# Kernel optimization log

Hardware: AMD Instinct MI355X
Metric: run time of the kernel (lower is better)

Reference implementation:

```python
import jax, jax.numpy as jnp
import numpy as np

N_SENT, B, S, D = 256, 512, 128, 1024
L, LATENT = 10331, 101  # int(sqrt(10331)) == 101


def setup_inputs() -> dict:
    key = jax.random.key(0)
    ks = jax.random.split(key, 16)
    inv = 1.0 / np.sqrt(D)
    return {
        'elmo_outputs': jax.random.normal(ks[0], (N_SENT, S, D), jnp.float32),
        'men_mask': jax.random.randint(ks[1], (B, S), 0, 2).astype(jnp.float32),
        'ctx_mask': jax.random.randint(ks[2], (B, S), 0, 2).astype(jnp.float32),
        'dist': jax.random.uniform(ks[3], (B, S), jnp.float32),
        'gathers': jax.random.randint(ks[4], (B,), 0, N_SENT),
        # nn.Linear weights, stored [out, in] as in torch
        'W_men_m': jax.random.normal(ks[5], (D, D), jnp.float32) * inv,
        'W_men_o': jax.random.normal(ks[6], (1, D), jnp.float32) * inv,
        'W_ctx_c': jax.random.normal(ks[7], (D, D), jnp.float32) * inv,
        'W_ctx_m': jax.random.normal(ks[8], (D, D), jnp.float32) * inv,
        'w_ctx_d': jax.random.normal(ks[9], (D,), jnp.float32),  # Linear(1, D) weight [D,1] squeezed
        'W_ctx_o': jax.random.normal(ks[10], (1, D), jnp.float32) * inv,
        'W_out': jax.random.normal(ks[11], (L, 2 * D), jnp.float32) * (1.0 / np.sqrt(2 * D)),
        'W_f2l': jax.random.normal(ks[12], (LATENT, 2 * D), jnp.float32) * (1.0 / np.sqrt(2 * D)),
        'W_l2l': jax.random.normal(ks[13], (L, LATENT), jnp.float32) * (1.0 / np.sqrt(LATENT)),
        'latent_scalar': jnp.array(0.1, jnp.float32),
    }


def reference(elmo_outputs, men_mask, ctx_mask, dist, gathers,
              W_men_m, W_men_o, W_ctx_c, W_ctx_m, w_ctx_d, W_ctx_o,
              W_out, W_f2l, W_l2l, latent_scalar):
    NEG = -10000.0
    # gather: sentence reps -> mention rows, [B, S, D]
    x = elmo_outputs[gathers]
    # mention additive attention
    men_h = jnp.tanh(jnp.einsum('bsd,ed->bse', x, W_men_m))
    men_score = jnp.einsum('bse,oe->bso', men_h, W_men_o)  # [B,S,1]
    men_score = men_score + (1.0 - men_mask[:, :, None]) * NEG
    men_attn = jax.nn.softmax(men_score, axis=1)
    men_repr = jnp.sum(x * men_attn, axis=1)  # [B, D]
    # context additive attention (dropout layers are identity in eval)
    ctx_h = jnp.tanh(
        jnp.einsum('bsd,ed->bse', x, W_ctx_c)
        + jnp.einsum('bd,ed->be', men_repr, W_ctx_m)[:, None, :]
        + dist[:, :, None] * w_ctx_d
    )
    ctx_score = jnp.einsum('bse,oe->bso', ctx_h, W_ctx_o)
    ctx_score = ctx_score + (1.0 - ctx_mask[:, :, None]) * NEG
    ctx_attn = jax.nn.softmax(ctx_score, axis=1)
    ctx_repr = jnp.sum(x * ctx_attn, axis=1)  # [B, D]
    final_repr = jnp.concatenate([men_repr, ctx_repr], axis=1)  # [B, 2D]
    outputs = final_repr @ W_out.T  # [B, L]
    latent_label = final_repr @ W_f2l.T  # [B, latent]
    outputs_latent = latent_label @ W_l2l.T  # [B, L]
    outputs = outputs + latent_scalar * outputs_latent
    return outputs, outputs_latent
```

## Files before the change

### kernel.cpp

```cpp
#include <hip/hip_runtime.h>
#include <hip/hip_bf16.h>

typedef __bf16 bf16x8 __attribute__((ext_vector_type(8)));
typedef float f32x4 __attribute__((ext_vector_type(4)));
typedef unsigned short u16x8 __attribute__((ext_vector_type(8)));

#define DEV __device__ __forceinline__

static constexpr int N_SENTC = 256, BB = 512, SS = 128, DD = 1024;
static constexpr int LL = 10331, LATENT = 101;
static constexpr int LPAD = 10368;
static constexpr int LATPAD = 128;

DEV float bf2f(unsigned short u) {
  unsigned v = (unsigned)u << 16;
  return __builtin_bit_cast(float, v);
}
DEV unsigned short f2bf(float f) {
  unsigned u = __builtin_bit_cast(unsigned, f);
  unsigned lsb = (u >> 16) & 1u;
  u += 0x7fffu + lsb;
  return (unsigned short)(u >> 16);
}

DEV void stage8(unsigned short* dst, const float* src) {
  float4 a = *(const float4*)src;
  float4 b = *(const float4*)(src + 4);
  unsigned short t[8];
  t[0] = f2bf(a.x); t[1] = f2bf(a.y); t[2] = f2bf(a.z); t[3] = f2bf(a.w);
  t[4] = f2bf(b.x); t[5] = f2bf(b.y); t[6] = f2bf(b.z); t[7] = f2bf(b.w);
  *(uint4*)dst = *(uint4*)t;
}

DEV void gl_lds16(const unsigned short* g, unsigned short* l) {
  __builtin_amdgcn_global_load_lds(
      (const __attribute__((address_space(1))) unsigned int*)g,
      (__attribute__((address_space(3))) unsigned int*)l, 16, 0, 0);
}

__global__ __launch_bounds__(256) void k_cvt(
    const float* __restrict__ src, unsigned short* __restrict__ dst, int n4) {
  for (int i = blockIdx.x * 256 + threadIdx.x; i < n4; i += gridDim.x * 256) {
    float4 v = ((const float4*)src)[i];
    unsigned short t[4] = {f2bf(v.x), f2bf(v.y), f2bf(v.z), f2bf(v.w)};
    ((uint2*)dst)[i] = *(const uint2*)t;
  }
}

__global__ __launch_bounds__(256) void k_cvt_pad(
    const float* __restrict__ src, unsigned short* __restrict__ dst,
    int srcR, int srcC, int dstC, int total) {
  for (int i = blockIdx.x * 256 + threadIdx.x; i < total; i += gridDim.x * 256) {
    int r = i / dstC, c = i - r * dstC;
    dst[i] = (r < srcR && c < srcC) ? f2bf(src[(size_t)r * srcC + c]) : (unsigned short)0;
  }
}

__global__ __launch_bounds__(256) void k_mc_gemm(
    const unsigned short* __restrict__ Xb, const unsigned short* __restrict__ Wmb,
    const unsigned short* __restrict__ Wcb, const float* __restrict__ wo,
    float* __restrict__ score, unsigned short* __restrict__ Hc) {
  __shared__ __align__(16) unsigned short As[128 * 32];
  __shared__ __align__(16) unsigned short Bs[128 * 32];
  const int colTile = blockIdx.x;
  const int rowBase = blockIdx.y * 128;
  const bool isMen = colTile < 8;
  const unsigned short* __restrict__ Bsrc = isMen ? Wmb : Wcb;
  const int bcolBase = (isMen ? colTile : colTile - 8) * 128;
  const int tid = threadIdx.x, wave = tid >> 6, lane = tid & 63;
  const int lm = lane & 15, lq = lane >> 4;
  const int wr = (wave & 1) * 64, wc = (wave >> 1) * 64;
  const int srow = wave * 32 + (lane >> 2);
  const int scol = (lane & 3) * 8;
  const unsigned short* aPtr = Xb + (size_t)(rowBase + srow) * 1024 + scol;
  const unsigned short* bPtr = Bsrc + (size_t)(bcolBase + srow) * 1024 + scol;
  unsigned short* aLds0 = As + wave * 1024;
  unsigned short* aLds1 = As + wave * 1024 + 512;
  unsigned short* bLds0 = Bs + wave * 1024;
  unsigned short* bLds1 = Bs + wave * 1024 + 512;
  f32x4 acc[4][4] = {};
  for (int k0 = 0; k0 < 1024; k0 += 32) {
    __syncthreads();
    gl_lds16(aPtr + k0, aLds0);
    gl_lds16(aPtr + k0 + 16 * 1024, aLds1);
    gl_lds16(bPtr + k0, bLds0);
    gl_lds16(bPtr + k0 + 16 * 1024, bLds1);
    __syncthreads();
    bf16x8 af[4], bfr[4];
#pragma unroll
    for (int m = 0; m < 4; ++m)
      af[m] = *(const bf16x8*)&As[(wr + m * 16 + lm) * 32 + lq * 8];
#pragma unroll
    for (int n = 0; n < 4; ++n)
      bfr[n] = *(const bf16x8*)&Bs[(wc + n * 16 + lm) * 32 + lq * 8];
#pragma unroll
    for (int m = 0; m < 4; ++m)
#pragma unroll
      for (int n = 0; n < 4; ++n)
        acc[m][n] = __builtin_amdgcn_mfma_f32_16x16x32_bf16(af[m], bfr[n], acc[m][n], 0, 0, 0);
  }
  if (isMen) {
    float wov[4];
#pragma unroll
    for (int n = 0; n < 4; ++n) wov[n] = wo[bcolBase + wc + n * 16 + lm];
    float rsum[4][4];
#pragma unroll
    for (int m = 0; m < 4; ++m)
#pragma unroll
      for (int r = 0; r < 4; ++r) {
        float s = 0.f;
#pragma unroll
        for (int n = 0; n < 4; ++n) s += tanhf(acc[m][n][r]) * wov[n];
        rsum[m][r] = s;
      }
#pragma unroll
    for (int msk = 1; msk <= 8; msk <<= 1)
#pragma unroll
      for (int m = 0; m < 4; ++m)
#pragma unroll
        for (int r = 0; r < 4; ++r) rsum[m][r] += __shfl_xor(rsum[m][r], msk, 64);
    if (lm == 0) {
#pragma unroll
      for (int m = 0; m < 4; ++m)
#pragma unroll
        for (int r = 0; r < 4; ++r)
          atomicAdd(&score[rowBase + wr + m * 16 + lq * 4 + r], rsum[m][r]);
    }
  } else {
#pragma unroll
    for (int m = 0; m < 4; ++m)
#pragma unroll
      for (int n = 0; n < 4; ++n) {
        int col = bcolBase + wc + n * 16 + lm;
#pragma unroll
        for (int r = 0; r < 4; ++r) {
          int row = rowBase + wr + m * 16 + lq * 4 + r;
          Hc[(size_t)row * 1024 + col] = f2bf(acc[m][n][r]);
        }
      }
  }
}

__global__ __launch_bounds__(256) void k_ctx_score(
    const unsigned short* __restrict__ Hc, const int* __restrict__ gathers,
    const float* __restrict__ cb, const float* __restrict__ wd,
    const float* __restrict__ wo, const float* __restrict__ dist,
    float* __restrict__ score) {
  const int b = blockIdx.x, tid = threadIdx.x, wave = tid >> 6, lane = tid & 63;
  const int n = gathers[b];
  __shared__ float cbl[1024], wdl[1024], wol[1024];
  for (int i = tid; i < 1024; i += 256) {
    cbl[i] = cb[b * 1024 + i];
    wdl[i] = wd[i];
    wol[i] = wo[i];
  }
  __syncthreads();
  for (int s = wave; s < 128; s += 4) {
    float d = dist[b * 128 + s];
    const unsigned short* hrow = &Hc[(size_t)(n * 128 + s) * 1024 + lane * 16];
    unsigned short hs[16];
    *(uint4*)hs = *(const uint4*)hrow;
    *(uint4*)(hs + 8) = *(const uint4*)(hrow + 8);
    float p = 0.f;
#pragma unroll
    for (int j = 0; j < 16; ++j) {
      int e = lane * 16 + j;
      p += tanhf(bf2f(hs[j]) + cbl[e] + d * wdl[e]) * wol[e];
    }
#pragma unroll
    for (int msk = 1; msk <= 32; msk <<= 1) p += __shfl_xor(p, msk, 64);
    if (lane == 0) score[b * 128 + s] = p;
  }
}

__global__ __launch_bounds__(256) void k_softb(
    const float* __restrict__ score_src, const float* __restrict__ mask,
    const unsigned short* __restrict__ Xb, const int* __restrict__ gathers,
    unsigned short* __restrict__ finalrb, int isCtx) {
  const int b = blockIdx.x, tid = threadIdx.x;
  const int n = gathers[b];
  __shared__ float attn[128];
  __shared__ float red[128 * 8];
  __shared__ float smax, ssum;
  if (tid < 128) {
    int srow = isCtx ? b : n;
    attn[tid] = score_src[srow * 128 + tid] + (1.0f - mask[b * 128 + tid]) * (-10000.0f);
  }
  __syncthreads();
  if (tid == 0) {
    float m = attn[0];
    for (int i = 1; i < 128; ++i) m = fmaxf(m, attn[i]);
    smax = m;
  }
  __syncthreads();
  if (tid < 128) attn[tid] = expf(attn[tid] - smax);
  __syncthreads();
  if (tid == 0) {
    float s = 0.f;
    for (int i = 0; i < 128; ++i) s += attn[i];
    ssum = 1.0f / s;
  }
  __syncthreads();
  if (tid < 128) attn[tid] *= ssum;
  __syncthreads();
  const unsigned short* xb = Xb + (size_t)n * 128 * 1024;
  const int c = tid & 127, h = tid >> 7;
  float acc[8] = {};
  for (int s = h; s < 128; s += 2) {
    float w = attn[s];
    u16x8 v = *(const u16x8*)&xb[(size_t)s * 1024 + c * 8];
#pragma unroll
    for (int j = 0; j < 8; ++j) acc[j] += w * bf2f(v[j]);
  }
  if (h == 1) {
#pragma unroll
    for (int j = 0; j < 8; ++j) red[c * 8 + j] = acc[j];
  }
  __syncthreads();
  if (h == 0) {
    unsigned short o[8];
#pragma unroll
    for (int j = 0; j < 8; ++j) o[j] = f2bf(acc[j] + red[c * 8 + j]);
    *(uint4*)&finalrb[(size_t)b * 2048 + (isCtx ? 1024 : 0) + c * 8] = *(uint4*)o;
  }
}

__global__ __launch_bounds__(256) void k_cb_gemm_b(
    const unsigned short* __restrict__ finalrb, const unsigned short* __restrict__ Wcmb,
    float* __restrict__ cb) {
  __shared__ __align__(16) unsigned short As[64 * 32];
  __shared__ __align__(16) unsigned short Bs[64 * 32];
  const int bid = blockIdx.x;
  const int rowBase = (bid >> 4) * 64, colBase = (bid & 15) * 64;
  const int tid = threadIdx.x, wave = tid >> 6, lane = tid & 63;
  const int lm = lane & 15, lq = lane >> 4;
  const int sr = tid >> 2, sc = (tid & 3) * 8;
  f32x4 acc[4] = {};
  for (int k0 = 0; k0 < 1024; k0 += 32) {
    __syncthreads();
    *(uint4*)&As[sr * 32 + sc] = *(const uint4*)&finalrb[(size_t)(rowBase + sr) * 2048 + k0 + sc];
    *(uint4*)&Bs[sr * 32 + sc] = *(const uint4*)&Wcmb[(size_t)(colBase + sr) * 1024 + k0 + sc];
    __syncthreads();
    bf16x8 af = *(const bf16x8*)&As[(wave * 16 + lm) * 32 + lq * 8];
#pragma unroll
    for (int j = 0; j < 4; ++j) {
      bf16x8 bfr = *(const bf16x8*)&Bs[(j * 16 + lm) * 32 + lq * 8];
      acc[j] = __builtin_amdgcn_mfma_f32_16x16x32_bf16(af, bfr, acc[j], 0, 0, 0);
    }
  }
#pragma unroll
  for (int j = 0; j < 4; ++j) {
    int col = colBase + j * 16 + lm;
#pragma unroll
    for (int r = 0; r < 4; ++r) {
      int row = rowBase + wave * 16 + lq * 4 + r;
      cb[row * 1024 + col] = acc[j][r];
    }
  }
}

__global__ __launch_bounds__(256) void k_lat_gemm_b(
    const unsigned short* __restrict__ finalrb, const unsigned short* __restrict__ Wf2lb,
    unsigned short* __restrict__ latb) {
  __shared__ __align__(16) unsigned short As[64 * 32];
  __shared__ __align__(16) unsigned short Bs[64 * 32];
  const int rowBase = blockIdx.y * 64, colBase = blockIdx.x * 64;
  const int tid = threadIdx.x, wave = tid >> 6, lane = tid & 63;
  const int lm = lane & 15, lq = lane >> 4;
  const int sr = tid >> 2, sc = (tid & 3) * 8;
  f32x4 acc[4] = {};
  for (int k0 = 0; k0 < 2048; k0 += 32) {
    __syncthreads();
    *(uint4*)&As[sr * 32 + sc] = *(const uint4*)&finalrb[(size_t)(rowBase + sr) * 2048 + k0 + sc];
    *(uint4*)&Bs[sr * 32 + sc] = *(const uint4*)&Wf2lb[(size_t)(colBase + sr) * 2048 + k0 + sc];
    __syncthreads();
    bf16x8 af = *(const bf16x8*)&As[(wave * 16 + lm) * 32 + lq * 8];
#pragma unroll
    for (int j = 0; j < 4; ++j) {
      bf16x8 bfr = *(const bf16x8*)&Bs[(j * 16 + lm) * 32 + lq * 8];
      acc[j] = __builtin_amdgcn_mfma_f32_16x16x32_bf16(af, bfr, acc[j], 0, 0, 0);
    }
  }
#pragma unroll
  for (int j = 0; j < 4; ++j) {
    int col = colBase + j * 16 + lm;
#pragma unroll
    for (int r = 0; r < 4; ++r) {
      int row = rowBase + wave * 16 + lq * 4 + r;
      latb[row * LATPAD + col] = f2bf(acc[j][r]);
    }
  }
}

__global__ __launch_bounds__(256) void k_out_gemm_b(
    const unsigned short* __restrict__ finalrb, const unsigned short* __restrict__ Woutb,
    const unsigned short* __restrict__ latb, const unsigned short* __restrict__ Wl2lb,
    const float* __restrict__ lscale, float* __restrict__ out,
    float* __restrict__ outLat) {
  __shared__ __align__(16) unsigned short As[64 * 32];
  __shared__ __align__(16) unsigned short Bs[64 * 32];
  const int rowBase = blockIdx.y * 64, colBase = blockIdx.x * 64;
  const int tid = threadIdx.x, wave = tid >> 6, lane = tid & 63;
  const int lm = lane & 15, lq = lane >> 4;
  const int sr = tid >> 2, sc = (tid & 3) * 8;
  const float scal = lscale[0];
  f32x4 acc[4] = {};
  for (int k0 = 0; k0 < 2048; k0 += 32) {
    __syncthreads();
    *(uint4*)&As[sr * 32 + sc] = *(const uint4*)&finalrb[(size_t)(rowBase + sr) * 2048 + k0 + sc];
    *(uint4*)&Bs[sr * 32 + sc] = *(const uint4*)&Woutb[(size_t)(colBase + sr) * 2048 + k0 + sc];
    __syncthreads();
    bf16x8 af = *(const bf16x8*)&As[(wave * 16 + lm) * 32 + lq * 8];
#pragma unroll
    for (int j = 0; j < 4; ++j) {
      bf16x8 bfr = *(const bf16x8*)&Bs[(j * 16 + lm) * 32 + lq * 8];
      acc[j] = __builtin_amdgcn_mfma_f32_16x16x32_bf16(af, bfr, acc[j], 0, 0, 0);
    }
  }
  f32x4 acc2[4] = {};
  for (int k2 = 0; k2 < 128; k2 += 32) {
    __syncthreads();
    *(uint4*)&As[sr * 32 + sc] = *(const uint4*)&latb[(size_t)(rowBase + sr) * LATPAD + k2 + sc];
    *(uint4*)&Bs[sr * 32 + sc] = *(const uint4*)&Wl2lb[(size_t)(colBase + sr) * LATPAD + k2 + sc];
    __syncthreads();
    bf16x8 af = *(const bf16x8*)&As[(wave * 16 + lm) * 32 + lq * 8];
#pragma unroll
    for (int j = 0; j < 4; ++j) {
      bf16x8 bfr = *(const bf16x8*)&Bs[(j * 16 + lm) * 32 + lq * 8];
      acc2[j] = __builtin_amdgcn_mfma_f32_16x16x32_bf16(af, bfr, acc2[j], 0, 0, 0);
    }
  }
#pragma unroll
  for (int j = 0; j < 4; ++j) {
    int col = colBase + j * 16 + lm;
    if (col < LL) {
#pragma unroll
      for (int r = 0; r < 4; ++r) {
        int row = rowBase + wave * 16 + lq * 4 + r;
        float lv = acc2[j][r];
        out[(size_t)row * LL + col] = acc[j][r] + scal * lv;
        outLat[(size_t)row * LL + col] = lv;
      }
    }
  }
}

__global__ __launch_bounds__(256) void k_men_gemm(
    const float* __restrict__ X, const float* __restrict__ Wm,
    const float* __restrict__ wo, float* __restrict__ score) {
  __shared__ __align__(16) unsigned short As[64 * 32];
  __shared__ __align__(16) unsigned short Bs[64 * 32];
  const int bid = blockIdx.x;
  const int rowBase = (bid >> 4) * 64, colBase = (bid & 15) * 64;
  const int tid = threadIdx.x, wave = tid >> 6, lane = tid & 63;
  const int lm = lane & 15, lq = lane >> 4;
  const int sr = tid >> 2, sc = (tid & 3) * 8;
  f32x4 acc[4] = {};
  for (int k0 = 0; k0 < 1024; k0 += 32) {
    __syncthreads();
    stage8(&As[sr * 32 + sc], &X[(size_t)(rowBase + sr) * 1024 + k0 + sc]);
    stage8(&Bs[sr * 32 + sc], &Wm[(size_t)(colBase + sr) * 1024 + k0 + sc]);
    __syncthreads();
    bf16x8 af = *(const bf16x8*)&As[(wave * 16 + lm) * 32 + lq * 8];
#pragma unroll
    for (int j = 0; j < 4; ++j) {
      bf16x8 bfr = *(const bf16x8*)&Bs[(j * 16 + lm) * 32 + lq * 8];
      acc[j] = __builtin_amdgcn_mfma_f32_16x16x32_bf16(af, bfr, acc[j], 0, 0, 0);
    }
  }
  float rsum[4] = {0.f, 0.f, 0.f, 0.f};
#pragma unroll
  for (int j = 0; j < 4; ++j) {
    float w = wo[colBase + j * 16 + lm];
#pragma unroll
    for (int r = 0; r < 4; ++r) rsum[r] += tanhf(acc[j][r]) * w;
  }
#pragma unroll
  for (int m = 1; m <= 8; m <<= 1)
#pragma unroll
    for (int r = 0; r < 4; ++r) rsum[r] += __shfl_xor(rsum[r], m, 64);
  if (lm == 0) {
    int row0 = rowBase + wave * 16 + lq * 4;
#pragma unroll
    for (int r = 0; r < 4; ++r) atomicAdd(&score[row0 + r], rsum[r]);
  }
}

__global__ __launch_bounds__(256) void k_ctx_gemm(
    const float* __restrict__ X, const int* __restrict__ gathers,
    const float* __restrict__ Wc, const float* __restrict__ wd,
    const float* __restrict__ wo, const float* __restrict__ dist,
    const float* __restrict__ cb, float* __restrict__ score) {
  __shared__ __align__(16) unsigned short As[64 * 32];
  __shared__ __align__(16) unsigned short Bs[64 * 32];
  const int bid = blockIdx.x;
  const int rowBase = (bid >> 4) * 64, colBase = (bid & 15) * 64;
  const int tid = threadIdx.x, wave = tid >> 6, lane = tid & 63;
  const int lm = lane & 15, lq = lane >> 4;
  const int sr = tid >> 2, sc = (tid & 3) * 8;
  const int row_g = rowBase + sr;
  const int srcRow = (gathers[row_g >> 7] << 7) + (row_g & 127);
  f32x4 acc[4] = {};
  for (int k0 = 0; k0 < 1024; k0 += 32) {
    __syncthreads();
    stage8(&As[sr * 32 + sc], &X[(size_t)srcRow * 1024 + k0 + sc]);
    stage8(&Bs[sr * 32 + sc], &Wc[(size_t)(colBase + sr) * 1024 + k0 + sc]);
    __syncthreads();
    bf16x8 af = *(const bf16x8*)&As[(wave * 16 + lm) * 32 + lq * 8];
#pragma unroll
    for (int j = 0; j < 4; ++j) {
      bf16x8 bfr = *(const bf16x8*)&Bs[(j * 16 + lm) * 32 + lq * 8];
      acc[j] = __builtin_amdgcn_mfma_f32_16x16x32_bf16(af, bfr, acc[j], 0, 0, 0);
    }
  }
  float rsum[4] = {0.f, 0.f, 0.f, 0.f};
#pragma unroll
  for (int j = 0; j < 4; ++j) {
    int col = colBase + j * 16 + lm;
    float w = wo[col];
    float wdv = wd[col];
#pragma unroll
    for (int r = 0; r < 4; ++r) {
      int rg = rowBase + wave * 16 + lq * 4 + r;
      int b = rg >> 7, s = rg & 127;
      float v = acc[j][r] + cb[b * 1024 + col] + dist[b * 128 + s] * wdv;
      rsum[r] += tanhf(v) * w;
    }
  }
#pragma unroll
  for (int m = 1; m <= 8; m <<= 1)
#pragma unroll
    for (int r = 0; r < 4; ++r) rsum[r] += __shfl_xor(rsum[r], m, 64);
  if (lm == 0) {
    int row0 = rowBase + wave * 16 + lq * 4;
#pragma unroll
    for (int r = 0; r < 4; ++r) atomicAdd(&score[row0 + r], rsum[r]);
  }
}

__global__ __launch_bounds__(256) void k_soft(
    const float* __restrict__ score_src, const float* __restrict__ mask,
    const float* __restrict__ X, const int* __restrict__ gathers,
    float* __restrict__ finalr, int isCtx) {
  const int b = blockIdx.x, tid = threadIdx.x;
  const int n = gathers[b];
  __shared__ float attn[128];
  __shared__ float smax, ssum;
  if (tid < 128) {
    int srow = isCtx ? b : n;
    attn[tid] = score_src[srow * 128 + tid] + (1.0f - mask[b * 128 + tid]) * (-10000.0f);
  }
  __syncthreads();
  if (tid == 0) {
    float m = attn[0];
    for (int i = 1; i < 128; ++i) m = fmaxf(m, attn[i]);
    smax = m;
  }
  __syncthreads();
  if (tid < 128) attn[tid] = expf(attn[tid] - smax);
  __syncthreads();
  if (tid == 0) {
    float s = 0.f;
    for (int i = 0; i < 128; ++i) s += attn[i];
    ssum = 1.0f / s;
  }
  __syncthreads();
  if (tid < 128) attn[tid] *= ssum;
  __syncthreads();
  const float* xb = &X[(size_t)(n << 7) * 1024];
  const int off = isCtx ? 1024 : 0;
  for (int d = tid; d < 1024; d += 256) {
    float a = 0.f;
#pragma unroll 8
    for (int s = 0; s < 128; ++s) a += attn[s] * xb[s * 1024 + d];
    finalr[b * 2048 + off + d] = a;
  }
}

__global__ __launch_bounds__(256) void k_cb_gemm(
    const float* __restrict__ finalr, const float* __restrict__ Wcm,
    float* __restrict__ cb) {
  __shared__ __align__(16) unsigned short As[64 * 32];
  __shared__ __align__(16) unsigned short Bs[64 * 32];
  const int bid = blockIdx.x;
  const int rowBase = (bid >> 4) * 64, colBase = (bid & 15) * 64;
  const int tid = threadIdx.x, wave = tid >> 6, lane = tid & 63;
  const int lm = lane & 15, lq = lane >> 4;
  const int sr = tid >> 2, sc = (tid & 3) * 8;
  f32x4 acc[4] = {};
  for (int k0 = 0; k0 < 1024; k0 += 32) {
    __syncthreads();
    stage8(&As[sr * 32 + sc], &finalr[(size_t)(rowBase + sr) * 2048 + k0 + sc]);
    stage8(&Bs[sr * 32 + sc], &Wcm[(size_t)(colBase + sr) * 1024 + k0 + sc]);
    __syncthreads();
    bf16x8 af = *(const bf16x8*)&As[(wave * 16 + lm) * 32 + lq * 8];
#pragma unroll
    for (int j = 0; j < 4; ++j) {
      bf16x8 bfr = *(const bf16x8*)&Bs[(j * 16 + lm) * 32 + lq * 8];
      acc[j] = __builtin_amdgcn_mfma_f32_16x16x32_bf16(af, bfr, acc[j], 0, 0, 0);
    }
  }
#pragma unroll
  for (int j = 0; j < 4; ++j) {
    int col = colBase + j * 16 + lm;
#pragma unroll
    for (int r = 0; r < 4; ++r) {
      int row = rowBase + wave * 16 + lq * 4 + r;
      cb[row * 1024 + col] = acc[j][r];
    }
  }
}

__global__ __launch_bounds__(256) void k_lat_gemm(
    const float* __restrict__ finalr, const float* __restrict__ Wf2l,
    float* __restrict__ lat) {
  __shared__ __align__(16) unsigned short As[64 * 32];
  __shared__ __align__(16) unsigned short Bs[64 * 32];
  const int rowBase = blockIdx.y * 64, colBase = blockIdx.x * 64;
  const int tid = threadIdx.x, wave = tid >> 6, lane = tid & 63;
  const int lm = lane & 15, lq = lane >> 4;
  const int sr = tid >> 2, sc = (tid & 3) * 8;
  f32x4 acc[4] = {};
  for (int k0 = 0; k0 < 2048; k0 += 32) {
    __syncthreads();
    stage8(&As[sr * 32 + sc], &finalr[(size_t)(rowBase + sr) * 2048 + k0 + sc]);
    int l = colBase + sr;
    if (l < LATENT) {
      stage8(&Bs[sr * 32 + sc], &Wf2l[(size_t)l * 2048 + k0 + sc]);
    } else {
      uint4 z = {0, 0, 0, 0};
      *(uint4*)&Bs[sr * 32 + sc] = z;
    }
    __syncthreads();
    bf16x8 af = *(const bf16x8*)&As[(wave * 16 + lm) * 32 + lq * 8];
#pragma unroll
    for (int j = 0; j < 4; ++j) {
      bf16x8 bfr = *(const bf16x8*)&Bs[(j * 16 + lm) * 32 + lq * 8];
      acc[j] = __builtin_amdgcn_mfma_f32_16x16x32_bf16(af, bfr, acc[j], 0, 0, 0);
    }
  }
#pragma unroll
  for (int j = 0; j < 4; ++j) {
    int col = colBase + j * 16 + lm;
    if (col < LATENT) {
#pragma unroll
      for (int r = 0; r < 4; ++r) {
        int row = rowBase + wave * 16 + lq * 4 + r;
        lat[row * LATENT + col] = acc[j][r];
      }
    }
  }
}

__global__ __launch_bounds__(256) void k_out_gemm(
    const float* __restrict__ finalr, const float* __restrict__ Wout,
    const float* __restrict__ lat, const float* __restrict__ Wl2l,
    const float* __restrict__ lscale, float* __restrict__ out,
    float* __restrict__ outLat) {
  __shared__ __align__(16) unsigned short As[64 * 32];
  __shared__ __align__(16) unsigned short Bs[64 * 32];
  const int rowBase = blockIdx.y * 64, colBase = blockIdx.x * 64;
  const int tid = threadIdx.x, wave = tid >> 6, lane = tid & 63;
  const int lm = lane & 15, lq = lane >> 4;
  const int sr = tid >> 2, sc = (tid & 3) * 8;
  const float scal = lscale[0];
  const int lrow = colBase + sr;
  const bool lvalid = (lrow < LL);
  f32x4 acc[4] = {};
  for (int k0 = 0; k0 < 2048; k0 += 32) {
    __syncthreads();
    stage8(&As[sr * 32 + sc], &finalr[(size_t)(rowBase + sr) * 2048 + k0 + sc]);
    if (lvalid) {
      stage8(&Bs[sr * 32 + sc], &Wout[(size_t)lrow * 2048 + k0 + sc]);
    } else {
      uint4 z = {0, 0, 0, 0};
      *(uint4*)&Bs[sr * 32 + sc] = z;
    }
    __syncthreads();
    bf16x8 af = *(const bf16x8*)&As[(wave * 16 + lm) * 32 + lq * 8];
#pragma unroll
    for (int j = 0; j < 4; ++j) {
      bf16x8 bfr = *(const bf16x8*)&Bs[(j * 16 + lm) * 32 + lq * 8];
      acc[j] = __builtin_amdgcn_mfma_f32_16x16x32_bf16(af, bfr, acc[j], 0, 0, 0);
    }
  }
  f32x4 acc2[4] = {};
  for (int k2 = 0; k2 < 128; k2 += 32) {
    __syncthreads();
    const int brow = rowBase + sr;
#pragma unroll
    for (int jj = 0; jj < 8; ++jj) {
      int idx = k2 + sc + jj;
      As[sr * 32 + sc + jj] = (idx < LATENT) ? f2bf(lat[brow * LATENT + idx]) : (unsigned short)0;
      Bs[sr * 32 + sc + jj] = (lvalid && idx < LATENT) ? f2bf(Wl2l[lrow * LATENT + idx]) : (unsigned short)0;
    }
    __syncthreads();
    bf16x8 af = *(const bf16x8*)&As[(wave * 16 + lm) * 32 + lq * 8];
#pragma unroll
    for (int j = 0; j < 4; ++j) {
      bf16x8 bfr = *(const bf16x8*)&Bs[(j * 16 + lm) * 32 + lq * 8];
      acc2[j] = __builtin_amdgcn_mfma_f32_16x16x32_bf16(af, bfr, acc2[j], 0, 0, 0);
    }
  }
#pragma unroll
  for (int j = 0; j < 4; ++j) {
    int col = colBase + j * 16 + lm;
    if (col < LL) {
#pragma unroll
      for (int r = 0; r < 4; ++r) {
        int row = rowBase + wave * 16 + lq * 4 + r;
        float lv = acc2[j][r];
        out[(size_t)row * LL + col] = acc[j][r] + scal * lv;
        outLat[(size_t)row * LL + col] = lv;
      }
    }
  }
}

extern "C" void kernel_launch(void* const* d_in, const int* in_sizes, int n_in,
                              void* d_out, int out_size, void* d_ws, size_t ws_size,
                              hipStream_t stream) {
  const float* X = (const float*)d_in[0];
  const float* men_mask = (const float*)d_in[1];
  const float* ctx_mask = (const float*)d_in[2];
  const float* dist = (const float*)d_in[3];
  const int* gathers = (const int*)d_in[4];
  const float* W_men_m = (const float*)d_in[5];
  const float* W_men_o = (const float*)d_in[6];
  const float* W_ctx_c = (const float*)d_in[7];
  const float* W_ctx_m = (const float*)d_in[8];
  const float* w_ctx_d = (const float*)d_in[9];
  const float* W_ctx_o = (const float*)d_in[10];
  const float* W_out = (const float*)d_in[11];
  const float* W_f2l = (const float*)d_in[12];
  const float* W_l2l = (const float*)d_in[13];
  const float* lscale = (const float*)d_in[14];
  float* out = (float*)d_out;
  float* outLat = out + (size_t)BB * LL;

  size_t off = 0;
  auto carve = [&](size_t bytes) {
    void* p = (char*)d_ws + off;
    off = (off + bytes + 255) & ~(size_t)255;
    return p;
  };
  float* sent_score = (float*)carve(32768 * 4);
  float* ctx_score = (float*)carve(65536 * 4);
  float* finalr = (float*)carve((size_t)512 * 2048 * 4);
  float* cb = (float*)carve((size_t)512 * 1024 * 4);
  float* lat = (float*)carve((size_t)512 * LATENT * 4);
  unsigned short* Xb = (unsigned short*)carve((size_t)32768 * 1024 * 2);
  unsigned short* Wmb = (unsigned short*)carve((size_t)1024 * 1024 * 2);
  unsigned short* Wcb = (unsigned short*)carve((size_t)1024 * 1024 * 2);
  unsigned short* Wcmb = (unsigned short*)carve((size_t)1024 * 1024 * 2);
  unsigned short* Hc = (unsigned short*)carve((size_t)32768 * 1024 * 2);
  unsigned short* Wf2lb = (unsigned short*)carve((size_t)LATPAD * 2048 * 2);
  unsigned short* Wl2lb = (unsigned short*)carve((size_t)LPAD * LATPAD * 2);
  unsigned short* finalrb = (unsigned short*)carve((size_t)512 * 2048 * 2);
  unsigned short* latb = (unsigned short*)carve((size_t)512 * LATPAD * 2);
  const bool fits = off <= ws_size;
  unsigned short* Woutb = Xb;

  if (fits) {
    hipMemsetAsync(sent_score, 0, 32768 * sizeof(float), stream);
    k_cvt<<<8192, 256, 0, stream>>>(X, Xb, 32768 * 1024 / 4);
    k_cvt<<<1024, 256, 0, stream>>>(W_men_m, Wmb, 1024 * 1024 / 4);
    k_cvt<<<1024, 256, 0, stream>>>(W_ctx_c, Wcb, 1024 * 1024 / 4);
    k_cvt<<<1024, 256, 0, stream>>>(W_ctx_m, Wcmb, 1024 * 1024 / 4);
    k_cvt<<<256, 256, 0, stream>>>(W_f2l, Wf2lb, LATENT * 2048 / 4);
    hipMemsetAsync(Wf2lb + (size_t)LATENT * 2048, 0,
                   (size_t)(LATPAD - LATENT) * 2048 * 2, stream);
    k_cvt_pad<<<1024, 256, 0, stream>>>(W_l2l, Wl2lb, LL, LATENT, LATPAD, LPAD * LATPAD);
    k_mc_gemm<<<dim3(16, 256), 256, 0, stream>>>(Xb, Wmb, Wcb, W_men_o, sent_score, Hc);
    k_softb<<<512, 256, 0, stream>>>(sent_score, men_mask, Xb, gathers, finalrb, 0);
    k_cb_gemm_b<<<128, 256, 0, stream>>>(finalrb, Wcmb, cb);
    k_ctx_score<<<512, 256, 0, stream>>>(Hc, gathers, cb, w_ctx_d, W_ctx_o, dist, ctx_score);
    k_softb<<<512, 256, 0, stream>>>(ctx_score, ctx_mask, Xb, gathers, finalrb, 1);
    k_lat_gemm_b<<<dim3(2, 8), 256, 0, stream>>>(finalrb, Wf2lb, latb);
    k_cvt<<<8192, 256, 0, stream>>>(W_out, Woutb, LL * 2048 / 4);
    hipMemsetAsync(Woutb + (size_t)LL * 2048, 0,
                   (size_t)(LPAD - LL) * 2048 * 2, stream);
    k_out_gemm_b<<<dim3(162, 8), 256, 0, stream>>>(finalrb, Woutb, latb, Wl2lb,
                                                   lscale, out, outLat);
  } else {
    hipMemsetAsync(d_ws, 0, (32768 + 65536) * sizeof(float), stream);
    k_men_gemm<<<8192, 256, 0, stream>>>(X, W_men_m, W_men_o, sent_score);
    k_soft<<<512, 256, 0, stream>>>(sent_score, men_mask, X, gathers, finalr, 0);
    k_cb_gemm<<<128, 256, 0, stream>>>(finalr, W_ctx_m, cb);
    k_ctx_gemm<<<16384, 256, 0, stream>>>(X, gathers, W_ctx_c, w_ctx_d, W_ctx_o, dist, cb, ctx_score);
    k_soft<<<512, 256, 0, stream>>>(ctx_score, ctx_mask, X, gathers, finalr, 1);
    k_lat_gemm<<<dim3(2, 8), 256, 0, stream>>>(finalr, W_f2l, lat);
    k_out_gemm<<<dim3(162, 8), 256, 0, stream>>>(finalr, W_out, lat, W_l2l, lscale, out, outLat);
  }
}
```

Measured before the change: 773.4 us.

## Deepen K-step in mc GEMM, retile output GEMM to 128x128, fuse pad conversions

The mention/context GEMM now loads two 32-wide K slices per barrier pair, which halves the number of synchronizations. The output GEMM is rewritten from 64x64 tiles with plain loads to 128x128 tiles using direct global-to-LDS loads, a 4x4 MFMA block per wave and the same 64-wide K step. That raises operand reuse and cuts the block count from 162x8 to 81x4. The separate convert and memset launches for W_f2l and W_out are merged into single k_cvt_pad launches. The trade-offs are higher register and LDS use per block and fewer blocks to fill the GPU, and the scalar k_cvt_pad conversion of the large W_out may be slower than the vectorized conversion it replaces.

```diff
diff --git a/kernel.cpp b/kernel.cpp
--- a/kernel.cpp
+++ b/kernel.cpp
@@ -60,8 +60,8 @@
     const unsigned short* __restrict__ Xb, const unsigned short* __restrict__ Wmb,
     const unsigned short* __restrict__ Wcb, const float* __restrict__ wo,
     float* __restrict__ score, unsigned short* __restrict__ Hc) {
-  __shared__ __align__(16) unsigned short As[128 * 32];
-  __shared__ __align__(16) unsigned short Bs[128 * 32];
+  __shared__ __align__(16) unsigned short As[2 * 128 * 32];
+  __shared__ __align__(16) unsigned short Bs[2 * 128 * 32];
   const int colTile = blockIdx.x;
   const int rowBase = blockIdx.y * 128;
   const bool isMen = colTile < 8;
@@ -74,30 +74,32 @@
   const int scol = (lane & 3) * 8;
   const unsigned short* aPtr = Xb + (size_t)(rowBase + srow) * 1024 + scol;
   const unsigned short* bPtr = Bsrc + (size_t)(bcolBase + srow) * 1024 + scol;
-  unsigned short* aLds0 = As + wave * 1024;
-  unsigned short* aLds1 = As + wave * 1024 + 512;
-  unsigned short* bLds0 = Bs + wave * 1024;
-  unsigned short* bLds1 = Bs + wave * 1024 + 512;
   f32x4 acc[4][4] = {};
-  for (int k0 = 0; k0 < 1024; k0 += 32) {
-    __syncthreads();
-    gl_lds16(aPtr + k0, aLds0);
-    gl_lds16(aPtr + k0 + 16 * 1024, aLds1);
-    gl_lds16(bPtr + k0, bLds0);
-    gl_lds16(bPtr + k0 + 16 * 1024, bLds1);
-    __syncthreads();
-    bf16x8 af[4], bfr[4];
-#pragma unroll
-    for (int m = 0; m < 4; ++m)
-      af[m] = *(const bf16x8*)&As[(wr + m * 16 + lm) * 32 + lq * 8];
-#pragma unroll
-    for (int n = 0; n < 4; ++n)
-      bfr[n] = *(const bf16x8*)&Bs[(wc + n * 16 + lm) * 32 + lq * 8];
-#pragma unroll
-    for (int m = 0; m < 4; ++m)
+  for (int k0 = 0; k0 < 1024; k0 += 64) {
+    __syncthreads();
+#pragma unroll
+    for (int h = 0; h < 2; ++h) {
+      gl_lds16(aPtr + k0 + h * 32, As + h * 4096 + wave * 1024);
+      gl_lds16(aPtr + k0 + h * 32 + 16 * 1024, As + h * 4096 + wave * 1024 + 512);
+      gl_lds16(bPtr + k0 + h * 32, Bs + h * 4096 + wave * 1024);
+      gl_lds16(bPtr + k0 + h * 32 + 16 * 1024, Bs + h * 4096 + wave * 1024 + 512);
+    }
+    __syncthreads();
+#pragma unroll
+    for (int h = 0; h < 2; ++h) {
+      bf16x8 af[4], bfr[4];
+#pragma unroll
+      for (int m = 0; m < 4; ++m)
+        af[m] = *(const bf16x8*)&As[h * 4096 + (wr + m * 16 + lm) * 32 + lq * 8];
 #pragma unroll
       for (int n = 0; n < 4; ++n)
-        acc[m][n] = __builtin_amdgcn_mfma_f32_16x16x32_bf16(af[m], bfr[n], acc[m][n], 0, 0, 0);
+        bfr[n] = *(const bf16x8*)&Bs[h * 4096 + (wc + n * 16 + lm) * 32 + lq * 8];
+#pragma unroll
+      for (int m = 0; m < 4; ++m)
+#pragma unroll
+        for (int n = 0; n < 4; ++n)
+          acc[m][n] = __builtin_amdgcn_mfma_f32_16x16x32_bf16(af[m], bfr[n], acc[m][n], 0, 0, 0);
+    }
   }
   if (isMen) {
     float wov[4];
@@ -297,52 +299,89 @@
     const unsigned short* __restrict__ latb, const unsigned short* __restrict__ Wl2lb,
     const float* __restrict__ lscale, float* __restrict__ out,
     float* __restrict__ outLat) {
-  __shared__ __align__(16) unsigned short As[64 * 32];
-  __shared__ __align__(16) unsigned short Bs[64 * 32];
-  const int rowBase = blockIdx.y * 64, colBase = blockIdx.x * 64;
-  const int tid = threadIdx.x, wave = tid >> 6, lane = tid & 63;
-  const int lm = lane & 15, lq = lane >> 4;
-  const int sr = tid >> 2, sc = (tid & 3) * 8;
+  __shared__ __align__(16) unsigned short As[2 * 128 * 32];
+  __shared__ __align__(16) unsigned short Bs[2 * 128 * 32];
+  const int colBase = blockIdx.x * 128;
+  const int rowBase = blockIdx.y * 128;
+  const int tid = threadIdx.x, wave = tid >> 6, lane = tid & 63;
+  const int lm = lane & 15, lq = lane >> 4;
+  const int wr = (wave & 1) * 64, wc = (wave >> 1) * 64;
+  const int srow = wave * 32 + (lane >> 2);
+  const int scol = (lane & 3) * 8;
   const float scal = lscale[0];
-  f32x4 acc[4] = {};
-  for (int k0 = 0; k0 < 2048; k0 += 32) {
-    __syncthreads();
-    *(uint4*)&As[sr * 32 + sc] = *(const uint4*)&finalrb[(size_t)(rowBase + sr) * 2048 + k0 + sc];
-    *(uint4*)&Bs[sr * 32 + sc] = *(const uint4*)&Woutb[(size_t)(colBase + sr) * 2048 + k0 + sc];
-    __syncthreads();
-    bf16x8 af = *(const bf16x8*)&As[(wave * 16 + lm) * 32 + lq * 8];
-#pragma unroll
-    for (int j = 0; j < 4; ++j) {
-      bf16x8 bfr = *(const bf16x8*)&Bs[(j * 16 + lm) * 32 + lq * 8];
-      acc[j] = __builtin_amdgcn_mfma_f32_16x16x32_bf16(af, bfr, acc[j], 0, 0, 0);
-    }
-  }
-  f32x4 acc2[4] = {};
-  for (int k2 = 0; k2 < 128; k2 += 32) {
-    __syncthreads();
-    *(uint4*)&As[sr * 32 + sc] = *(const uint4*)&latb[(size_t)(rowBase + sr) * LATPAD + k2 + sc];
-    *(uint4*)&Bs[sr * 32 + sc] = *(const uint4*)&Wl2lb[(size_t)(colBase + sr) * LATPAD + k2 + sc];
-    __syncthreads();
-    bf16x8 af = *(const bf16x8*)&As[(wave * 16 + lm) * 32 + lq * 8];
-#pragma unroll
-    for (int j = 0; j < 4; ++j) {
-      bf16x8 bfr = *(const bf16x8*)&Bs[(j * 16 + lm) * 32 + lq * 8];
-      acc2[j] = __builtin_amdgcn_mfma_f32_16x16x32_bf16(af, bfr, acc2[j], 0, 0, 0);
-    }
-  }
-#pragma unroll
-  for (int j = 0; j < 4; ++j) {
-    int col = colBase + j * 16 + lm;
-    if (col < LL) {
-#pragma unroll
-      for (int r = 0; r < 4; ++r) {
-        int row = rowBase + wave * 16 + lq * 4 + r;
-        float lv = acc2[j][r];
-        out[(size_t)row * LL + col] = acc[j][r] + scal * lv;
-        outLat[(size_t)row * LL + col] = lv;
+  const unsigned short* aPtr = finalrb + (size_t)(rowBase + srow) * 2048 + scol;
+  const unsigned short* bPtr = Woutb + (size_t)(colBase + srow) * 2048 + scol;
+  f32x4 acc[4][4] = {};
+  for (int k0 = 0; k0 < 2048; k0 += 64) {
+    __syncthreads();
+#pragma unroll
+    for (int h = 0; h < 2; ++h) {
+      gl_lds16(aPtr + k0 + h * 32, As + h * 4096 + wave * 1024);
+      gl_lds16(aPtr + k0 + h * 32 + 16 * 2048, As + h * 4096 + wave * 1024 + 512);
+      gl_lds16(bPtr + k0 + h * 32, Bs + h * 4096 + wave * 1024);
+      gl_lds16(bPtr + k0 + h * 32 + 16 * 2048, Bs + h * 4096 + wave * 1024 + 512);
+    }
+    __syncthreads();
+#pragma unroll
+    for (int h = 0; h < 2; ++h) {
+      bf16x8 af[4], bfr[4];
+#pragma unroll
+      for (int m = 0; m < 4; ++m)
+        af[m] = *(const bf16x8*)&As[h * 4096 + (wr + m * 16 + lm) * 32 + lq * 8];
+#pragma unroll
+      for (int n = 0; n < 4; ++n)
+        bfr[n] = *(const bf16x8*)&Bs[h * 4096 + (wc + n * 16 + lm) * 32 + lq * 8];
+#pragma unroll
+      for (int m = 0; m < 4; ++m)
+#pragma unroll
+        for (int n = 0; n < 4; ++n)
+          acc[m][n] = __builtin_amdgcn_mfma_f32_16x16x32_bf16(af[m], bfr[n], acc[m][n], 0, 0, 0);
+    }
+  }
+  const unsigned short* aPtr2 = latb + (size_t)(rowBase + srow) * LATPAD + scol;
+  const unsigned short* bPtr2 = Wl2lb + (size_t)(colBase + srow) * LATPAD + scol;
+  f32x4 acc2[4][4] = {};
+  for (int k0 = 0; k0 < 128; k0 += 64) {
+    __syncthreads();
+#pragma unroll
+    for (int h = 0; h < 2; ++h) {
+      gl_lds16(aPtr2 + k0 + h * 32, As + h * 4096 + wave * 1024);
+      gl_lds16(aPtr2 + k0 + h * 32 + 16 * LATPAD, As + h * 4096 + wave * 1024 + 512);
+      gl_lds16(bPtr2 + k0 + h * 32, Bs + h * 4096 + wave * 1024);
+      gl_lds16(bPtr2 + k0 + h * 32 + 16 * LATPAD, Bs + h * 4096 + wave * 1024 + 512);
+    }
+    __syncthreads();
+#pragma unroll
+    for (int h = 0; h < 2; ++h) {
+      bf16x8 af[4], bfr[4];
+#pragma unroll
+      for (int m = 0; m < 4; ++m)
+        af[m] = *(const bf16x8*)&As[h * 4096 + (wr + m * 16 + lm) * 32 + lq * 8];
+#pragma unroll
+      for (int n = 0; n < 4; ++n)
+        bfr[n] = *(const bf16x8*)&Bs[h * 4096 + (wc + n * 16 + lm) * 32 + lq * 8];
+#pragma unroll
+      for (int m = 0; m < 4; ++m)
+#pragma unroll
+        for (int n = 0; n < 4; ++n)
+          acc2[m][n] = __builtin_amdgcn_mfma_f32_16x16x32_bf16(af[m], bfr[n], acc2[m][n], 0, 0, 0);
+    }
+  }
+#pragma unroll
+  for (int m = 0; m < 4; ++m)
+#pragma unroll
+    for (int n = 0; n < 4; ++n) {
+      int col = colBase + wc + n * 16 + lm;
+      if (col < LL) {
+#pragma unroll
+        for (int r = 0; r < 4; ++r) {
+          int row = rowBase + wr + m * 16 + lq * 4 + r;
+          float lv = acc2[m][n][r];
+          out[(size_t)row * LL + col] = acc[m][n][r] + scal * lv;
+          outLat[(size_t)row * LL + col] = lv;
+        }
       }
     }
-  }
 }
 
 __global__ __launch_bounds__(256) void k_men_gemm(
@@ -667,9 +706,7 @@
     k_cvt<<<1024, 256, 0, stream>>>(W_men_m, Wmb, 1024 * 1024 / 4);
     k_cvt<<<1024, 256, 0, stream>>>(W_ctx_c, Wcb, 1024 * 1024 / 4);
     k_cvt<<<1024, 256, 0, stream>>>(W_ctx_m, Wcmb, 1024 * 1024 / 4);
-    k_cvt<<<256, 256, 0, stream>>>(W_f2l, Wf2lb, LATENT * 2048 / 4);
-    hipMemsetAsync(Wf2lb + (size_t)LATENT * 2048, 0,
-                   (size_t)(LATPAD - LATENT) * 2048 * 2, stream);
+    k_cvt_pad<<<512, 256, 0, stream>>>(W_f2l, Wf2lb, LATENT, 2048, 2048, LATPAD * 2048);
     k_cvt_pad<<<1024, 256, 0, stream>>>(W_l2l, Wl2lb, LL, LATENT, LATPAD, LPAD * LATPAD);
     k_mc_gemm<<<dim3(16, 256), 256, 0, stream>>>(Xb, Wmb, Wcb, W_men_o, sent_score, Hc);
     k_softb<<<512, 256, 0, stream>>>(sent_score, men_mask, Xb, gathers, finalrb, 0);
@@ -677,11 +714,9 @@
     k_ctx_score<<<512, 256, 0, stream>>>(Hc, gathers, cb, w_ctx_d, W_ctx_o, dist, ctx_score);
     k_softb<<<512, 256, 0, stream>>>(ctx_score, ctx_mask, Xb, gathers, finalrb, 1);
     k_lat_gemm_b<<<dim3(2, 8), 256, 0, stream>>>(finalrb, Wf2lb, latb);
-    k_cvt<<<8192, 256, 0, stream>>>(W_out, Woutb, LL * 2048 / 4);
-    hipMemsetAsync(Woutb + (size_t)LL * 2048, 0,
-                   (size_t)(LPAD - LL) * 2048 * 2, stream);
-    k_out_gemm_b<<<dim3(162, 8), 256, 0, stream>>>(finalrb, Woutb, latb, Wl2lb,
-                                                   lscale, out, outLat);
+    k_cvt_pad<<<8192, 256, 0, stream>>>(W_out, Woutb, LL, 2048, 2048, LPAD * 2048);
+    k_out_gemm_b<<<dim3(81, 4), 256, 0, stream>>>(finalrb, Woutb, latb, Wl2lb,
+                                                  lscale, out, outLat);
   } else {
     hipMemsetAsync(d_ws, 0, (32768 + 65536) * sizeof(float), stream);
     k_men_gemm<<<8192, 256, 0, stream>>>(X, W_men_m, W_men_o, sent_score);
```

Measured after the change: 740.9 us. 1.04x faster.
